# Optimization experiments

Measured on AMD Instinct MI355X. Metric: run time of the kernel, lower is better.

Reference implementation:

```python
import jax, jax.numpy as jnp
import numpy as np

WINDOW = 129  # must be odd; matches init_kwargs


def setup_inputs() -> dict:
    key = jax.random.key(0)
    kq, kk, kv = jax.random.split(key, 3)
    shape = (1, 2048, 8, 64)  # (b, s, nh, h)
    return {
        "q": jax.random.normal(kq, shape, dtype=jnp.float32),
        "k": jax.random.normal(kk, shape, dtype=jnp.float32),
        "v": jax.random.normal(kv, shape, dtype=jnp.float32),
    }


def reference(q, k, v):
    # Sliding-window local attention, faithful to the pad+unfold torch module.
    b, s, nh, h = k.shape
    w = (WINDOW - 1) // 2
    W = 2 * w + 1
    scale = h ** (-0.5)
    qn = q * scale

    # zero-pad keys/values along the sequence dim by w on both sides
    kp = jnp.pad(k, ((0, 0), (w, w), (0, 0), (0, 0)))  # (b, s+2w, nh, h)
    vp = jnp.pad(v, ((0, 0), (w, w), (0, 0), (0, 0)))

    # idx[j, q] = j + q : padded key position for window offset j at query q
    idx = jnp.arange(W)[:, None] + jnp.arange(s)[None, :]  # (W, s)
    kw = kp[:, idx]  # (b, W, s, nh, h) -- unfolded key windows
    vw = vp[:, idx]  # (b, W, s, nh, h)

    # A[b, q, j, n] = <q[b,q,n,:], k_padded[b, j+q, n, :]>
    A = jnp.einsum('bqnh,bjqnh->bqjn', qn, kw)

    # mask out window slots pointing at padding (key pos j+q-w outside [0, s))
    valid = (idx >= w) & (idx < s + w)  # (W, s)
    mask_value = -jnp.finfo(A.dtype).max
    A = jnp.where(valid.T[None, :, :, None], A, mask_value)  # (1, s, W, 1) bcast

    # softmax over the window-offset axis (dim=-2 in the torch module)
    A = jax.nn.softmax(A, axis=2)

    # z[b, q, n, h] = sum_j A[b,q,j,n] * v_padded[b, j+q, n, h]
    z = jnp.einsum('bqjn,bjqnh->bqnh', A, vw)
    return z
```

## Files before the change

kernel.cpp:

```cpp
#include <hip/hip_runtime.h>
#include <math.h>


typedef __attribute__((ext_vector_type(8))) short short8;
typedef __attribute__((ext_vector_type(4))) float f32x4;

namespace {
constexpr int SEQ = 2048, NH = 8, HD = 64, WHALF = 64;
constexpr int TQ  = 32;
constexpr int ROWS = 160;
constexpr int KST  = 72;
constexpr int PST  = 168;
constexpr int NHD  = NH * HD;
}

__device__ __forceinline__ ushort f2bf(float x) {
  return (ushort)((__float_as_uint(x) + 0x8000u) >> 16);
}
__device__ __forceinline__ float fexp2(float x) {
  float r;
  asm("v_exp_f32 %0, %1" : "=v"(r) : "v"(x));
  return r;
}
__device__ __forceinline__ float frcp(float x) {
  float r;
  asm("v_rcp_f32 %0, %1" : "=v"(r) : "v"(x));
  return r;
}

__global__ __launch_bounds__(512, 4) void wattn_kernel(
    const float* __restrict__ q, const float* __restrict__ k,
    const float* __restrict__ v, float* __restrict__ out) {
  __shared__ __align__(16) short sK[ROWS * KST];
  __shared__ __align__(16) short sQ[TQ * KST];
  __shared__ __align__(16) short sP[TQ * PST];
  __shared__ __align__(16) float sD[8 * 16];

  const int t = threadIdx.x;
  const int bid  = blockIdx.x;
  const int W    = (bid & 7) * 64 + (bid >> 3);
  const int tile = W & 63;
  const int n    = W >> 6;
  const int q0   = tile * TQ;
  const size_t hb = (size_t)n * HD;

  const int w = t >> 6, lane = t & 63, lq = lane & 15, lg = lane >> 4;
  const int qh = w & 1;
  const int ht = w >> 1;

  #pragma unroll
  for (int it = 0; it < 5; ++it) {
    int f = t + it * 512;
    int row = f >> 4, c16 = f & 15;
    int grow = q0 - WHALF + row;
    int cg = min(max(grow, 0), SEQ - 1);
    float4 kv = *(const float4*)(k + (size_t)cg * NHD + hb + c16 * 4);
    uint lo = (uint)f2bf(kv.x) | ((uint)f2bf(kv.y) << 16);
    uint hi = (uint)f2bf(kv.z) | ((uint)f2bf(kv.w) << 16);
    *(uint2*)&sK[row * KST + c16 * 4] = make_uint2(lo, hi);
  }
  {
    int row = t >> 4, c16 = t & 15;
    float4 qv = *(const float4*)(q + (size_t)(q0 + row) * NHD + hb + c16 * 4);
    uint lo = (uint)f2bf(qv.x) | ((uint)f2bf(qv.y) << 16);
    uint hi = (uint)f2bf(qv.z) | ((uint)f2bf(qv.w) << 16);
    *(uint2*)&sQ[row * KST + c16 * 4] = make_uint2(lo, hi);
  }

  const float* vcol = v + hb + ht * 16 + lq;
  float vf[5][8];
  #pragma unroll
  for (int kc = 0; kc < 5; ++kc)
    #pragma unroll
    for (int j = 0; j < 8; ++j) {
      int row  = kc * 32 + 8 * lg + j;
      int grow = q0 - WHALF + row;
      int cg   = min(max(grow, 0), SEQ - 1);
      vf[kc][j] = vcol[(size_t)cg * NHD];
    }

  __syncthreads();

  const int qd = qh * 16 + lq;
  const short8 qf0 = *(const short8*)&sQ[qd * KST + 8 * lg];
  const short8 qf1 = *(const short8*)&sQ[qd * KST + 32 + 8 * lg];

  const float EXPC = 0.125f * 1.4426950408889634f;
  const int rlo = max(qd, WHALF - q0);
  const int rhi = min(qd + 2 * WHALF, SEQ - 1 + WHALF - q0);

  auto do_tile = [&](int rt, float& ws) {
    const int rb = rt * 16;
    short8 kf0 = *(const short8*)&sK[(rb + lq) * KST + 8 * lg];
    short8 kf1 = *(const short8*)&sK[(rb + lq) * KST + 32 + 8 * lg];
    f32x4 acc = {0.f, 0.f, 0.f, 0.f};
    acc = __builtin_amdgcn_mfma_f32_16x16x32_bf16(kf0, qf0, acc, 0, 0, 0);
    acc = __builtin_amdgcn_mfma_f32_16x16x32_bf16(kf1, qf1, acc, 0, 0, 0);
    ushort pb[4];
    #pragma unroll
    for (int r = 0; r < 4; ++r) {
      int row = rb + 4 * lg + r;
      bool valid = (row >= rlo) && (row <= rhi);
      float p = valid ? fexp2((float)acc[r] * EXPC) : 0.f;
      ws += p;
      pb[r] = f2bf(p);
    }
    uint lo = (uint)pb[0] | ((uint)pb[1] << 16);
    uint hi = (uint)pb[2] | ((uint)pb[3] << 16);
    *(uint2*)&sP[qd * PST + rb + 4 * lg] = make_uint2(lo, hi);
  };

  float ws = 0.f;
  do_tile(ht, ws);
  do_tile(ht + 4, ws);
  if (w < 4) do_tile(8 + (w >> 1), ws);

  ws += __shfl_xor(ws, 16);
  ws += __shfl_xor(ws, 32);
  if (lane < 16) sD[w * 16 + lane] = ws;

  __syncthreads();

  float4 dsum = make_float4(0.f, 0.f, 0.f, 0.f);
  #pragma unroll
  for (int j = 0; j < 4; ++j) {
    float4 dp = *(const float4*)(sD + (qh + 2 * j) * 16 + 4 * lg);
    dsum.x += dp.x; dsum.y += dp.y; dsum.z += dp.z; dsum.w += dp.w;
  }
  short8 pa[5];
  #pragma unroll
  for (int kc = 0; kc < 5; ++kc)
    pa[kc] = *(const short8*)&sP[qd * PST + kc * 32 + 8 * lg];

  f32x4 acc = {0.f, 0.f, 0.f, 0.f};
  #pragma unroll
  for (int kc = 0; kc < 5; ++kc) {
    short8 vb;
    #pragma unroll
    for (int j = 0; j < 8; ++j) vb[j] = (short)f2bf(vf[kc][j]);
    acc = __builtin_amdgcn_mfma_f32_16x16x32_bf16(pa[kc], vb, acc, 0, 0, 0);
  }

  float di[4] = {frcp(dsum.x), frcp(dsum.y), frcp(dsum.z), frcp(dsum.w)};
  float* op = out + (size_t)(q0 + qh * 16 + 4 * lg) * NHD + hb + ht * 16 + lq;
  #pragma unroll
  for (int r = 0; r < 4; ++r)
    op[(size_t)r * NHD] = (float)acc[r] * di[r];
}

extern "C" void kernel_launch(void* const* d_in, const int* in_sizes, int n_in,
                              void* d_out, int out_size, void* d_ws, size_t ws_size,
                              hipStream_t stream) {
  const float* q = (const float*)d_in[0];
  const float* k = (const float*)d_in[1];
  const float* v = (const float*)d_in[2];
  float* out = (float*)d_out;
  dim3 grid((SEQ / TQ) * NH);
  hipLaunchKernelGGL(wattn_kernel, grid, dim3(512), 0, stream, q, k, v, out);
}
```

Before: 10.77 us.

## Split PV stage so half the waves handle both query halves

Work is repartitioned across the 8 waves. Waves 0-3 now load V for their 16-column slice and compute the PV MFMA for both 16-query halves, reusing each converted V fragment twice. Waves 4-7 take the extra QK tile that waves 0-3 used to do. This halves the V global loads and bf16 conversions per block and balances the QK stage against the PV stage, but it leaves half the waves idle in the final stage and puts more serial work on waves 0-3.

```diff
diff --git a/kernel.cpp b/kernel.cpp
--- a/kernel.cpp
+++ b/kernel.cpp
@@ -67,17 +67,19 @@
     *(uint2*)&sQ[row * KST + c16 * 4] = make_uint2(lo, hi);
   }
 
-  const float* vcol = v + hb + ht * 16 + lq;
   float vf[5][8];
-  #pragma unroll
-  for (int kc = 0; kc < 5; ++kc)
+  if (w < 4) {
+    const float* vcol = v + hb + w * 16 + lq;
     #pragma unroll
-    for (int j = 0; j < 8; ++j) {
-      int row  = kc * 32 + 8 * lg + j;
-      int grow = q0 - WHALF + row;
-      int cg   = min(max(grow, 0), SEQ - 1);
-      vf[kc][j] = vcol[(size_t)cg * NHD];
-    }
+    for (int kc = 0; kc < 5; ++kc)
+      #pragma unroll
+      for (int j = 0; j < 8; ++j) {
+        int row  = kc * 32 + 8 * lg + j;
+        int grow = q0 - WHALF + row;
+        int cg   = min(max(grow, 0), SEQ - 1);
+        vf[kc][j] = vcol[(size_t)cg * NHD];
+      }
+  }
 
   __syncthreads();
 
@@ -113,7 +115,7 @@
   float ws = 0.f;
   do_tile(ht, ws);
   do_tile(ht + 4, ws);
-  if (w < 4) do_tile(8 + (w >> 1), ws);
+  if (w >= 4) do_tile(8 + ((w - 4) >> 1), ws);
 
   ws += __shfl_xor(ws, 16);
   ws += __shfl_xor(ws, 32);
@@ -121,31 +123,40 @@
 
   __syncthreads();
 
-  float4 dsum = make_float4(0.f, 0.f, 0.f, 0.f);
-  #pragma unroll
-  for (int j = 0; j < 4; ++j) {
-    float4 dp = *(const float4*)(sD + (qh + 2 * j) * 16 + 4 * lg);
-    dsum.x += dp.x; dsum.y += dp.y; dsum.z += dp.z; dsum.w += dp.w;
+  if (w < 4) {
+    float4 d0 = make_float4(0.f, 0.f, 0.f, 0.f);
+    float4 d1 = make_float4(0.f, 0.f, 0.f, 0.f);
+    #pragma unroll
+    for (int j = 0; j < 4; ++j) {
+      float4 a = *(const float4*)(sD + (2 * j + 0) * 16 + 4 * lg);
+      float4 b = *(const float4*)(sD + (2 * j + 1) * 16 + 4 * lg);
+      d0.x += a.x; d0.y += a.y; d0.z += a.z; d0.w += a.w;
+      d1.x += b.x; d1.y += b.y; d1.z += b.z; d1.w += b.w;
+    }
+
+    f32x4 acc0 = {0.f, 0.f, 0.f, 0.f};
+    f32x4 acc1 = {0.f, 0.f, 0.f, 0.f};
+    #pragma unroll
+    for (int kc = 0; kc < 5; ++kc) {
+      short8 vb;
+      #pragma unroll
+      for (int j = 0; j < 8; ++j) vb[j] = (short)f2bf(vf[kc][j]);
+      short8 pa0 = *(const short8*)&sP[(lq)      * PST + kc * 32 + 8 * lg];
+      short8 pa1 = *(const short8*)&sP[(16 + lq) * PST + kc * 32 + 8 * lg];
+      acc0 = __builtin_amdgcn_mfma_f32_16x16x32_bf16(pa0, vb, acc0, 0, 0, 0);
+      acc1 = __builtin_amdgcn_mfma_f32_16x16x32_bf16(pa1, vb, acc1, 0, 0, 0);
+    }
+
+    float di0[4] = {frcp(d0.x), frcp(d0.y), frcp(d0.z), frcp(d0.w)};
+    float di1[4] = {frcp(d1.x), frcp(d1.y), frcp(d1.z), frcp(d1.w)};
+    float* op0 = out + (size_t)(q0 + 4 * lg) * NHD + hb + w * 16 + lq;
+    float* op1 = op0 + (size_t)16 * NHD;
+    #pragma unroll
+    for (int r = 0; r < 4; ++r) {
+      op0[(size_t)r * NHD] = (float)acc0[r] * di0[r];
+      op1[(size_t)r * NHD] = (float)acc1[r] * di1[r];
+    }
   }
-  short8 pa[5];
-  #pragma unroll
-  for (int kc = 0; kc < 5; ++kc)
-    pa[kc] = *(const short8*)&sP[qd * PST + kc * 32 + 8 * lg];
-
-  f32x4 acc = {0.f, 0.f, 0.f, 0.f};
-  #pragma unroll
-  for (int kc = 0; kc < 5; ++kc) {
-    short8 vb;
-    #pragma unroll
-    for (int j = 0; j < 8; ++j) vb[j] = (short)f2bf(vf[kc][j]);
-    acc = __builtin_amdgcn_mfma_f32_16x16x32_bf16(pa[kc], vb, acc, 0, 0, 0);
-  }
-
-  float di[4] = {frcp(dsum.x), frcp(dsum.y), frcp(dsum.z), frcp(dsum.w)};
-  float* op = out + (size_t)(q0 + qh * 16 + 4 * lg) * NHD + hb + ht * 16 + lq;
-  #pragma unroll
-  for (int r = 0; r < 4; ++r)
-    op[(size_t)r * NHD] = (float)acc[r] * di[r];
 }
 
 extern "C" void kernel_launch(void* const* d_in, const int* in_sizes, int n_in,
```

New measurement: 11.22 us. 1.04x slower.
